# Performance work log

Hardware: AMD Instinct MI355X
Metric: run time of the kernel (lower is better)

The kernel has to match this reference:

```python
import jax, jax.numpy as jnp
import numpy as np

NODE_CNT = 1_000_000
EMB_DIM = 128     # embedding_dim
H1 = 128          # hidden_dim_list[1] (leaf fc, linear, no bias)
H0 = 128          # hidden_dim_list[0] (root fc, sigmoid, bias)
B, N0, N1 = 1024, 25, 10


def setup_inputs() -> dict:
    key = jax.random.key(0)
    k1, k2, k3, k4, k5, k6, k7 = jax.random.split(key, 7)
    roots = jax.random.randint(k1, (B,), 0, NODE_CNT)
    idx1 = jax.random.randint(k2, (B, N0), 0, NODE_CNT)
    idx2 = jax.random.randint(k3, (B, N0, N1), 0, NODE_CNT)
    embed_table = jax.random.normal(k4, (NODE_CNT + 1, EMB_DIM), dtype=jnp.float32) * 0.05
    # fc1: last layer, input 2*EMB_DIM -> H1, no bias, linear
    W1 = jax.random.normal(k5, (2 * EMB_DIM, H1), dtype=jnp.float32) * 0.05
    # fc0: input EMB_DIM + H1 -> H0, bias, sigmoid
    W0 = jax.random.normal(k6, (EMB_DIM + H1, H0), dtype=jnp.float32) * 0.05
    b0 = jax.random.normal(k7, (H0,), dtype=jnp.float32) * 0.05
    return {"embed_table": embed_table, "W0": W0, "b0": b0, "W1": W1,
            "roots": roots, "idx1": idx1, "idx2": idx2}


def reference(embed_table, W0, b0, W1, roots, idx1, idx2):
    # Layer 1 (leaf): mean of sampled 2-hop neighbor embeddings
    leaf = embed_table[idx2]                      # [B, N0, N1, D]
    mean_leaf = jnp.mean(leaf, axis=-2)           # [B, N0, D]
    h1 = embed_table[idx1]                        # [B, N0, D]
    z1 = jnp.concatenate([h1, mean_leaf], axis=-1) @ W1   # [B, N0, H1] (linear, no bias)
    # Layer 0 (root): mean of layer-1 outputs over first-hop neighbors
    mean0 = jnp.mean(z1, axis=1)                  # [B, H1]
    h0 = embed_table[roots]                       # [B, D]
    out = jax.nn.sigmoid(jnp.concatenate([h0, mean0], axis=-1) @ W0 + b0)  # [B, H0]
    return out
```

## Files before the change

### kernel.cpp

```cpp
#include <hip/hip_runtime.h>

#define NBATCH 1024
#define N0     25
#define N1     10
#define NLEAF  (N0 * N1)
#define SPLITS 4

__global__ __launch_bounds__(256) void sage_gather(
    const float* __restrict__ emb,
    const int* __restrict__ idx1,
    const int* __restrict__ idx2,
    float* __restrict__ ws)
{
    const int blk  = blockIdx.x;
    const int b    = blk >> 2;
    const int s    = blk & 3;
    const int tid  = threadIdx.x;
    const int slot = tid >> 4;
    const int cc   = tid & 15;

    const int lstart = s * 63;
    const int lcnt   = (s == 3) ? (NLEAF - 3 * 63) : 63;
    const int istart = s * 7;
    const int icnt   = (s == 3) ? (N0 - 3 * 7) : 7;

    __shared__ int   sidx[80];
    __shared__ float red[16][128];

    if (tid < lcnt)                   sidx[tid]      = idx2[b * NLEAF + lstart + tid];
    if (tid >= 64 && tid < 64 + icnt) sidx[tid]      = idx1[b * N0 + istart + (tid - 64)];
    __syncthreads();

    const char* embb = (const char*)emb;
    const uint32_t coff = (uint32_t)cc * 32u;

    float acc[8];
#pragma unroll
    for (int j = 0; j < 8; ++j) acc[j] = 0.f;

#pragma unroll
    for (int i = 0; i < 3; ++i) {
        int id = sidx[slot + 16 * i];
        const float4* p = (const float4*)(embb + (uint32_t)id * 512u + coff);
        float4 v0 = p[0];
        float4 v1 = p[1];
        acc[0] += v0.x; acc[1] += v0.y; acc[2] += v0.z; acc[3] += v0.w;
        acc[4] += v1.x; acc[5] += v1.y; acc[6] += v1.z; acc[7] += v1.w;
    }
    if (slot + 48 < lcnt) {
        int id = sidx[slot + 48];
        const float4* p = (const float4*)(embb + (uint32_t)id * 512u + coff);
        float4 v0 = p[0];
        float4 v1 = p[1];
        acc[0] += v0.x; acc[1] += v0.y; acc[2] += v0.z; acc[3] += v0.w;
        acc[4] += v1.x; acc[5] += v1.y; acc[6] += v1.z; acc[7] += v1.w;
    }
#pragma unroll
    for (int j = 0; j < 8; ++j) red[slot][cc * 8 + j] = acc[j];
    __syncthreads();
    if (tid < 128) {
        float t = 0.f;
#pragma unroll
        for (int g = 0; g < 16; ++g) t += red[g][tid];
        ws[(size_t)blk * 256 + tid] = t;
    }
    __syncthreads();

#pragma unroll
    for (int j = 0; j < 8; ++j) acc[j] = 0.f;
    if (slot < icnt) {
        int id = sidx[64 + slot];
        const float4* p = (const float4*)(embb + (uint32_t)id * 512u + coff);
        float4 v0 = p[0];
        float4 v1 = p[1];
        acc[0] += v0.x; acc[1] += v0.y; acc[2] += v0.z; acc[3] += v0.w;
        acc[4] += v1.x; acc[5] += v1.y; acc[6] += v1.z; acc[7] += v1.w;
    }
#pragma unroll
    for (int j = 0; j < 8; ++j) red[slot][cc * 8 + j] = acc[j];
    __syncthreads();
    if (tid < 128) {
        float t = 0.f;
#pragma unroll
        for (int g = 0; g < 16; ++g) t += red[g][tid];
        ws[(size_t)blk * 256 + 128 + tid] = t;
    }
}

__global__ __launch_bounds__(256) void sage_finish(
    const float* __restrict__ emb,
    const float* __restrict__ W0,
    const float* __restrict__ b0,
    const float* __restrict__ W1,
    const int* __restrict__ roots,
    const float* __restrict__ ws,
    float* __restrict__ out)
{
    const int b   = blockIdx.x;
    const int tid = threadIdx.x;

    __shared__ float hr[128];
    __shared__ float m1[128];
    __shared__ float m2[128];
    __shared__ float tv[128];
    __shared__ float red2[2][128];

    const int root = roots[b];
    if (tid < 32) {
        float4 v = ((const float4*)((const char*)emb + (uint32_t)root * 512u))[tid];
        ((float4*)hr)[tid] = v;
    }

    {
        float p = 0.f;
#pragma unroll
        for (int s = 0; s < SPLITS; ++s) p += ws[(size_t)b * 1024 + s * 256 + tid];
        if (tid < 128) m2[tid] = p * (1.0f / NLEAF);
        else           m1[tid - 128] = p * (1.0f / N0);
    }
    __syncthreads();

    const int c = tid & 127;
    const int h = tid >> 7;

    {
        const float* xh = h ? m2 : m1;
        const float* w = W1 + (size_t)(h * 128) * 128 + c;
        float q = 0.f;
#pragma unroll 8
        for (int k = 0; k < 128; ++k) {
            q += xh[k] * w[(size_t)k * 128];
        }
        red2[h][c] = q;
    }
    __syncthreads();
    if (tid < 128) tv[tid] = red2[0][tid] + red2[1][tid];
    __syncthreads();

    {
        const float* yh = h ? tv : hr;
        const float* w = W0 + (size_t)(h * 128) * 128 + c;
        float q = 0.f;
#pragma unroll 8
        for (int k = 0; k < 128; ++k) {
            q += yh[k] * w[(size_t)k * 128];
        }
        red2[h][c] = q;
    }
    __syncthreads();
    if (tid < 128) {
        float z = red2[0][tid] + red2[1][tid] + b0[tid];
        float sg = 1.0f / (1.0f + __expf(-z));
        out[(size_t)b * 128 + tid] = sg;
    }
}

extern "C" void kernel_launch(void* const* d_in, const int* in_sizes, int n_in,
                              void* d_out, int out_size, void* d_ws, size_t ws_size,
                              hipStream_t stream) {
    const float* emb   = (const float*)d_in[0];
    const float* W0    = (const float*)d_in[1];
    const float* b0    = (const float*)d_in[2];
    const float* W1    = (const float*)d_in[3];
    const int*   roots = (const int*)d_in[4];
    const int*   idx1  = (const int*)d_in[5];
    const int*   idx2  = (const int*)d_in[6];
    float* out = (float*)d_out;
    float* ws  = (float*)d_ws;

    sage_gather<<<NBATCH * SPLITS, 256, 0, stream>>>(emb, idx1, idx2, ws);
    sage_finish<<<NBATCH, 256, 0, stream>>>(emb, W0, b0, W1, roots, ws, out);
}
```

Measured before the change: 598.8 us.

## Fuse gather and finish kernels into a single per-batch kernel

Replaces the split gather kernel plus finish kernel with one kernel per batch element. It gathers all leaf, first-hop and root rows with 32 lanes per row and an unrolled loop, then reduces in shared memory and runs the two matvecs in place. This removes the workspace write/read and the second launch. The cost is fewer blocks (one per batch element instead of four) and a longer serial gather loop per wave, which could reduce latency hiding.

```diff
diff --git a/kernel.cpp b/kernel.cpp
--- a/kernel.cpp
+++ b/kernel.cpp
@@ -4,119 +4,80 @@
 #define N0     25
 #define N1     10
 #define NLEAF  (N0 * N1)
-#define SPLITS 4
+#define NROWS  (NLEAF + N0 + 1)
 
-__global__ __launch_bounds__(256) void sage_gather(
-    const float* __restrict__ emb,
-    const int* __restrict__ idx1,
-    const int* __restrict__ idx2,
-    float* __restrict__ ws)
-{
-    const int blk  = blockIdx.x;
-    const int b    = blk >> 2;
-    const int s    = blk & 3;
-    const int tid  = threadIdx.x;
-    const int slot = tid >> 4;
-    const int cc   = tid & 15;
-
-    const int lstart = s * 63;
-    const int lcnt   = (s == 3) ? (NLEAF - 3 * 63) : 63;
-    const int istart = s * 7;
-    const int icnt   = (s == 3) ? (N0 - 3 * 7) : 7;
-
-    __shared__ int   sidx[80];
-    __shared__ float red[16][128];
-
-    if (tid < lcnt)                   sidx[tid]      = idx2[b * NLEAF + lstart + tid];
-    if (tid >= 64 && tid < 64 + icnt) sidx[tid]      = idx1[b * N0 + istart + (tid - 64)];
-    __syncthreads();
-
-    const char* embb = (const char*)emb;
-    const uint32_t coff = (uint32_t)cc * 32u;
-
-    float acc[8];
-#pragma unroll
-    for (int j = 0; j < 8; ++j) acc[j] = 0.f;
-
-#pragma unroll
-    for (int i = 0; i < 3; ++i) {
-        int id = sidx[slot + 16 * i];
-        const float4* p = (const float4*)(embb + (uint32_t)id * 512u + coff);
-        float4 v0 = p[0];
-        float4 v1 = p[1];
-        acc[0] += v0.x; acc[1] += v0.y; acc[2] += v0.z; acc[3] += v0.w;
-        acc[4] += v1.x; acc[5] += v1.y; acc[6] += v1.z; acc[7] += v1.w;
-    }
-    if (slot + 48 < lcnt) {
-        int id = sidx[slot + 48];
-        const float4* p = (const float4*)(embb + (uint32_t)id * 512u + coff);
-        float4 v0 = p[0];
-        float4 v1 = p[1];
-        acc[0] += v0.x; acc[1] += v0.y; acc[2] += v0.z; acc[3] += v0.w;
-        acc[4] += v1.x; acc[5] += v1.y; acc[6] += v1.z; acc[7] += v1.w;
-    }
-#pragma unroll
-    for (int j = 0; j < 8; ++j) red[slot][cc * 8 + j] = acc[j];
-    __syncthreads();
-    if (tid < 128) {
-        float t = 0.f;
-#pragma unroll
-        for (int g = 0; g < 16; ++g) t += red[g][tid];
-        ws[(size_t)blk * 256 + tid] = t;
-    }
-    __syncthreads();
-
-#pragma unroll
-    for (int j = 0; j < 8; ++j) acc[j] = 0.f;
-    if (slot < icnt) {
-        int id = sidx[64 + slot];
-        const float4* p = (const float4*)(embb + (uint32_t)id * 512u + coff);
-        float4 v0 = p[0];
-        float4 v1 = p[1];
-        acc[0] += v0.x; acc[1] += v0.y; acc[2] += v0.z; acc[3] += v0.w;
-        acc[4] += v1.x; acc[5] += v1.y; acc[6] += v1.z; acc[7] += v1.w;
-    }
-#pragma unroll
-    for (int j = 0; j < 8; ++j) red[slot][cc * 8 + j] = acc[j];
-    __syncthreads();
-    if (tid < 128) {
-        float t = 0.f;
-#pragma unroll
-        for (int g = 0; g < 16; ++g) t += red[g][tid];
-        ws[(size_t)blk * 256 + 128 + tid] = t;
-    }
-}
-
-__global__ __launch_bounds__(256) void sage_finish(
+__global__ __launch_bounds__(256) void sage_fused(
     const float* __restrict__ emb,
     const float* __restrict__ W0,
     const float* __restrict__ b0,
     const float* __restrict__ W1,
     const int* __restrict__ roots,
-    const float* __restrict__ ws,
+    const int* __restrict__ idx1,
+    const int* __restrict__ idx2,
     float* __restrict__ out)
 {
-    const int b   = blockIdx.x;
-    const int tid = threadIdx.x;
+    const int b    = blockIdx.x;
+    const int tid  = threadIdx.x;
+    const int slot = tid >> 5;
+    const int c4   = tid & 31;
 
+    __shared__ int   sidx[NROWS];
+    __shared__ float red[8][256];
     __shared__ float hr[128];
     __shared__ float m1[128];
     __shared__ float m2[128];
     __shared__ float tv[128];
     __shared__ float red2[2][128];
 
-    const int root = roots[b];
-    if (tid < 32) {
-        float4 v = ((const float4*)((const char*)emb + (uint32_t)root * 512u))[tid];
-        ((float4*)hr)[tid] = v;
+    if (tid < NLEAF) sidx[tid]         = idx2[b * NLEAF + tid];
+    if (tid < N0)    sidx[NLEAF + tid] = idx1[b * N0 + tid];
+    if (tid == 255)  sidx[NROWS - 1]   = roots[b];
+    __syncthreads();
+
+    const char* embb = (const char*)emb;
+    const uint32_t coff = (uint32_t)c4 * 16u;
+
+    float accL0 = 0.f, accL1 = 0.f, accL2 = 0.f, accL3 = 0.f;
+    float accI0 = 0.f, accI1 = 0.f, accI2 = 0.f, accI3 = 0.f;
+
+#pragma unroll 8
+    for (int i = 0; i < 31; ++i) {
+        int id = sidx[slot + 8 * i];
+        float4 v = *(const float4*)(embb + ((uint32_t)id * 512u + coff));
+        accL0 += v.x; accL1 += v.y; accL2 += v.z; accL3 += v.w;
     }
+#pragma unroll
+    for (int i = 31; i < 35; ++i) {
+        int k = slot + 8 * i;
+        if (k < NROWS) {
+            int id = sidx[k];
+            float4 v = *(const float4*)(embb + ((uint32_t)id * 512u + coff));
+            if (k < NLEAF) {
+                accL0 += v.x; accL1 += v.y; accL2 += v.z; accL3 += v.w;
+            } else if (k < NROWS - 1) {
+                accI0 += v.x; accI1 += v.y; accI2 += v.z; accI3 += v.w;
+            } else {
+                hr[c4 * 4 + 0] = v.x; hr[c4 * 4 + 1] = v.y;
+                hr[c4 * 4 + 2] = v.z; hr[c4 * 4 + 3] = v.w;
+            }
+        }
+    }
+    red[slot][c4 * 4 + 0] = accL0;
+    red[slot][c4 * 4 + 1] = accL1;
+    red[slot][c4 * 4 + 2] = accL2;
+    red[slot][c4 * 4 + 3] = accL3;
+    red[slot][128 + c4 * 4 + 0] = accI0;
+    red[slot][128 + c4 * 4 + 1] = accI1;
+    red[slot][128 + c4 * 4 + 2] = accI2;
+    red[slot][128 + c4 * 4 + 3] = accI3;
+    __syncthreads();
 
     {
-        float p = 0.f;
+        float s = 0.f;
 #pragma unroll
-        for (int s = 0; s < SPLITS; ++s) p += ws[(size_t)b * 1024 + s * 256 + tid];
-        if (tid < 128) m2[tid] = p * (1.0f / NLEAF);
-        else           m1[tid - 128] = p * (1.0f / N0);
+        for (int g = 0; g < 8; ++g) s += red[g][tid];
+        if (tid < 128) m2[tid] = s * (1.0f / NLEAF);
+        else           m1[tid - 128] = s * (1.0f / N0);
     }
     __syncthreads();
 
@@ -166,8 +127,6 @@
     const int*   idx1  = (const int*)d_in[5];
     const int*   idx2  = (const int*)d_in[6];
     float* out = (float*)d_out;
-    float* ws  = (float*)d_ws;
 
-    sage_gather<<<NBATCH * SPLITS, 256, 0, stream>>>(emb, idx1, idx2, ws);
-    sage_finish<<<NBATCH, 256, 0, stream>>>(emb, W0, b0, W1, roots, ws, out);
+    sage_fused<<<NBATCH, 256, 0, stream>>>(emb, W0, b0, W1, roots, idx1, idx2, out);
 }
```

New measurement: 590.9 us. Within noise of the previous version (-1.3%).
